# Kernel optimization log

Hardware: AMD Instinct MI355X
Metric: run time of the kernel (lower is better)

The kernel has to match this reference:

```python
import jax, jax.numpy as jnp
import numpy as np
from jax import lax

B, N, M = 4, 16384, 512
RADIUS2 = 4.0        # radius=2 (hard-coded in forward), compare squared distances
BALL_K = 64          # k=64 hard-coded in forward
KNN_K = 9            # opt.node_knn_k_1
SIGMA_LB = 0.001     # opt.loss_sigma_lower_bound

_DIMS = [("conv1", 6, 64), ("conv2", 64, 64), ("conv3", 64, 64),
         ("conv4", 128, 128), ("conv5", 128, 128),
         ("knnb1", 131, 256), ("knnb2", 256, 256), ("knnb3", 256, 256),
         ("knna1", 512, 512), ("knna2", 512, 512),
         ("mlp1", 640, 512), ("mlp2", 512, 256)]


def setup_inputs() -> dict:
    key = jax.random.key(0)
    ks = jax.random.split(key, 6)
    inp = {
        "x": jax.random.normal(ks[0], (B, 3, N), jnp.float32),
        "sn": jax.random.normal(ks[1], (B, 3, N), jnp.float32),
        "node": jax.random.normal(ks[2], (B, 3, M), jnp.float32),
    }
    for i, (name, cin, cout) in enumerate(_DIMS):
        k = jax.random.fold_in(ks[3], i)
        inp[name + "_w"] = jax.random.normal(k, (cout, cin), jnp.float32) * np.float32(1.0 / np.sqrt(cin))
        inp[name + "_b"] = jnp.zeros((cout,), jnp.float32)
    inp["mlp3_w"] = jax.random.normal(ks[4], (4, 256), jnp.float32) * np.float32(1e-4)  # .normal_(0, 0.0001)
    inp["mlp3_b"] = jnp.zeros((4,), jnp.float32)
    return inp


def _conv(f, w, b, act=True):
    # 1x1 conv over (B,C,M) or (B,C,M,K): channel matmul + bias (+relu)
    y = jnp.einsum('oc,bc...->bo...', w, f) + b.reshape((1, -1) + (1,) * (f.ndim - 2))
    return jax.nn.relu(y) if act else y


def _sqdist(a, b):
    # a: (B,3,Ma), b: (B,3,Nb) -> (B,Ma,Nb) squared euclidean distances
    aa = jnp.sum(a * a, axis=1)
    bb = jnp.sum(b * b, axis=1)
    ab = jnp.einsum('bcm,bcn->bmn', a, b)
    return aa[:, :, None] + bb[:, None, :] - 2.0 * ab


def _gather(feat, idx):
    # feat: (B,C,Nb), idx: (B,Mq,K) -> (B,C,Mq,K)
    Bq, C, _ = feat.shape
    _, Mq, K = idx.shape
    flat = jnp.broadcast_to(idx.reshape(Bq, 1, Mq * K), (Bq, C, Mq * K))
    return jnp.take_along_axis(feat, flat, axis=2).reshape(Bq, C, Mq, K)


def _ball_query(sqd, radius2, k):
    # first k point indices (in original order) with dist<radius, padded by the first hit
    n = sqd.shape[2]
    mask = sqd < radius2
    keyi = jnp.where(mask, jnp.arange(n, dtype=jnp.int32)[None, None, :], jnp.int32(n))
    _, idx = lax.top_k(-keyi, k)  # k smallest keys == first k in-ball indices
    count = jnp.sum(mask, axis=2, keepdims=True)
    return jnp.where(jnp.arange(k)[None, None, :] < count, idx, idx[:, :, :1])


def reference(x, sn, node,
              conv1_w, conv1_b, conv2_w, conv2_b, conv3_w, conv3_b,
              conv4_w, conv4_b, conv5_w, conv5_b,
              knnb1_w, knnb1_b, knnb2_w, knnb2_b, knnb3_w, knnb3_b,
              knna1_w, knna1_b, knna2_w, knna2_b,
              mlp1_w, mlp1_b, mlp2_w, mlp2_b, mlp3_w, mlp3_b):
    x_aug = jnp.concatenate([x, sn], axis=1)                      # (B,6,N)
    idx = _ball_query(_sqdist(node, x), RADIUS2, BALL_K)          # (B,M,64)
    xb = _gather(x_aug, idx)                                      # (B,6,M,64)
    xb = jnp.concatenate([xb[:, :3] - node[:, :, :, None], xb[:, 3:]], axis=1)
    f = _conv(_conv(_conv(xb, conv1_w, conv1_b), conv2_w, conv2_b), conv3_w, conv3_b)
    fmax = jnp.max(f, axis=3, keepdims=True)
    f = jnp.concatenate([f, jnp.broadcast_to(fmax, f.shape)], axis=1)
    f = _conv(_conv(f, conv4_w, conv4_b), conv5_w, conv5_b)
    feat1 = jnp.max(f, axis=3)                                    # (B,128,M)

    # GeneralKNNFusionModule: query=node, database=node, x=feat1, K=KNN_K
    _, knn_idx = lax.top_k(-_sqdist(node, node), KNN_K)           # (B,M,K) nearest nodes
    coords = _gather(node, knn_idx) - node[:, :, :, None]         # (B,3,M,K)
    g = jnp.concatenate([coords, _gather(feat1, knn_idx)], axis=1)  # (B,131,M,K)
    g = _conv(_conv(_conv(g, knnb1_w, knnb1_b), knnb2_w, knnb2_b), knnb3_w, knnb3_b)
    gmax = jnp.max(g, axis=3, keepdims=True)
    g = jnp.concatenate([g, jnp.broadcast_to(gmax, g.shape)], axis=1)
    g = _conv(_conv(g, knna1_w, knna1_b), knna2_w, knna2_b)
    feat2 = jnp.max(g, axis=3)                                    # (B,512,M)

    h = jnp.concatenate([feat1, feat2], axis=1)                   # (B,640,M)
    h = _conv(_conv(h, mlp1_w, mlp1_b), mlp2_w, mlp2_b)
    ksig = _conv(h, mlp3_w, mlp3_b, act=False)                    # (B,4,M)
    keypoints = ksig[:, :3] + node
    sigmas = jax.nn.softplus(ksig[:, 3]) + SIGMA_LB
    return node, keypoints, sigmas
```

## Files before the change

### kernel.cpp

```cpp
#include <hip/hip_runtime.h>

typedef unsigned short u16;
typedef unsigned int u32;
typedef __bf16 bf16x8 __attribute__((ext_vector_type(8)));
typedef float floatx4 __attribute__((ext_vector_type(4)));
typedef unsigned short u16x8 __attribute__((ext_vector_type(8)));
typedef unsigned int u32x4 __attribute__((ext_vector_type(4)));

static constexpr int B_ = 4;
static constexpr int N_ = 16384;
static constexpr int M_ = 512;

__device__ __forceinline__ u16 f2bf(float f) {
    u32 u = __float_as_uint(f);
    u32 r = (u + 0x7fffu + ((u >> 16) & 1u)) >> 16;
    return (u16)r;
}
__device__ __forceinline__ float bf2f(u16 x) {
    return __uint_as_float(((u32)x) << 16);
}
__device__ __forceinline__ u32 pack2(float a, float b) {
    return (u32)f2bf(a) | ((u32)f2bf(b) << 16);
}

struct WConvArgs { const float* src[12]; };

__global__ __launch_bounds__(256) void prep_kernel(
    const float* __restrict__ x, const float* __restrict__ node,
    int* __restrict__ idx, int* __restrict__ knn,
    WConvArgs wa, u16* __restrict__ Wbf) {
    int bid = blockIdx.x;
    int tid = threadIdx.x, wave = tid >> 6, lane = tid & 63;

    if (bid < 2048) {
        int bm = bid;
        int b = bm >> 9, m = bm & 511;
        __shared__ int sidx[4][64];
        __shared__ int scnt[4];
        const float* xb = x + (size_t)b * 3 * N_;
        float nx = node[((size_t)b * 3 + 0) * M_ + m];
        float ny = node[((size_t)b * 3 + 1) * M_ + m];
        float nz = node[((size_t)b * 3 + 2) * M_ + m];
        float aa = nx * nx + ny * ny + nz * nz;
        int cnt = 0;
        int base = wave * 4096;
        for (int n0 = base; n0 < base + 4096; n0 += 256) {
            float px[4], py[4], pz[4];
#pragma unroll
            for (int i = 0; i < 4; ++i) {
                int n = n0 + i * 64 + lane;
                px[i] = xb[n]; py[i] = xb[N_ + n]; pz[i] = xb[2 * N_ + n];
            }
#pragma unroll
            for (int i = 0; i < 4; ++i) {
                float bb = px[i] * px[i] + py[i] * py[i] + pz[i] * pz[i];
                float d = aa + bb - 2.0f * (nx * px[i] + ny * py[i] + nz * pz[i]);
                bool inb = d < 4.0f;
                unsigned long long mask = __ballot(inb);
                if (inb && cnt < 64) {
                    int pos = cnt + __popcll(mask & ((1ull << lane) - 1ull));
                    if (pos < 64) sidx[wave][pos] = n0 + i * 64 + lane;
                }
                cnt += __popcll(mask);
            }
            if (cnt >= 64) break;
        }
        if (lane == 0) scnt[wave] = cnt;
        __syncthreads();
        if (tid < 64) {
            int total = scnt[0] + scnt[1] + scnt[2] + scnt[3];
            int v = 0;
            if (total > 0) {
                int lim = total < 64 ? total : 64;
                int slot = tid < lim ? tid : 0;
                int w = 0, pre = 0;
                while (w < 3 && slot >= pre + scnt[w]) { pre += scnt[w]; ++w; }
                v = sidx[w][slot - pre];
            }
            idx[(size_t)bm * 64 + tid] = v;
        }
    } else if (bid < 2560) {
        int bm = (bid - 2048) * 4 + wave;
        int b = bm >> 9, m = bm & 511;
        const float* nb = node + (size_t)b * 3 * M_;
        float nx = nb[m], ny = nb[M_ + m], nz = nb[2 * M_ + m];
        float aa = nx * nx + ny * ny + nz * nz;
        float dist[8];
        int didx[8];
#pragma unroll
        for (int i = 0; i < 8; ++i) {
            int n = lane + i * 64;
            float px = nb[n], py = nb[M_ + n], pz = nb[2 * M_ + n];
            float bb = px * px + py * py + pz * pz;
            float ab = nx * px + ny * py + nz * pz;
            dist[i] = aa + bb - 2.0f * ab;
            didx[i] = n;
        }
        for (int r = 0; r < 9; ++r) {
            float bv = dist[0]; int bi = didx[0]; int bslot = 0;
#pragma unroll
            for (int i = 1; i < 8; ++i) {
                if (dist[i] < bv || (dist[i] == bv && didx[i] < bi)) {
                    bv = dist[i]; bi = didx[i]; bslot = i;
                }
            }
            float rv = bv; int ri = bi;
            for (int off = 32; off > 0; off >>= 1) {
                float ov = __shfl_down(rv, off);
                int   oi = __shfl_down(ri, off);
                if (ov < rv || (ov == rv && oi < ri)) { rv = ov; ri = oi; }
            }
            ri = __shfl(ri, 0);
            if (lane == 0) knn[(size_t)bm * 9 + r] = ri;
            if (bi == ri) dist[bslot] = 3.0e38f;
        }
    } else {
        const int CI[12] = {6, 64, 64, 128, 128, 131, 256, 256, 512, 512, 640, 512};
        const int KP[12] = {32, 64, 64, 128, 128, 160, 256, 256, 512, 512, 640, 512};
        const int OFF[13] = {0, 2048, 6144, 10240, 26624, 43008, 83968, 149504,
                             215040, 477184, 739328, 1067008, 1198080};
        int e = (bid - 2560) * 256 + tid;
        int w = 0;
        while (e >= OFF[w + 1]) ++w;
        int local = e - OFF[w];
        int kp = KP[w];
        int co = local / kp, k = local - co * kp;
        float v = 0.0f;
        if (w == 5) {
            if (k < 3) v = wa.src[5][(size_t)co * 131 + k];
            else if (k >= 8 && k < 136) v = wa.src[5][(size_t)co * 131 + (k - 5)];
        } else if (k < CI[w]) {
            v = wa.src[w][(size_t)co * CI[w] + k];
        }
        Wbf[e] = f2bf(v);
    }
}

static constexpr int RS = 136;

__device__ __forceinline__ bf16x8 ldsA(const u16* act, int rf, int l15, int quad, int ks) {
    return *(const bf16x8*)(act + (rf * 16 + l15) * RS + ks * 32 + quad * 8);
}
__device__ __forceinline__ bf16x8 ldW(const u16* W, int ks, int l15, int quad, int kstride) {
    return *(const bf16x8*)(W + (size_t)l15 * kstride + ks * 32 + quad * 8);
}

__global__ __launch_bounds__(256, 2) void fused_stage1_kernel(
    const float* __restrict__ x, const float* __restrict__ sn,
    const float* __restrict__ node, const int* __restrict__ idx,
    const u16* __restrict__ Wbf,
    const float* __restrict__ b1, const float* __restrict__ b2,
    const float* __restrict__ b3, const float* __restrict__ b4,
    const float* __restrict__ b5, u16* __restrict__ h) {
    __shared__ __align__(16) u16 act[256 * RS];
    __shared__ __align__(16) u16 mv[4][64];
    int blk = blockIdx.x;
    int bm0 = blk * 4;
    int tid = threadIdx.x, wave = tid >> 6, lane = tid & 63;
    int quad = lane >> 4, l15 = lane & 15;

    {
        int row = tid;
        int bm = bm0 + (row >> 6);
        int b = bm >> 9, m = bm & 511;
        int j = idx[(size_t)bm * 64 + (row & 63)];
        const float* xb = x + (size_t)b * 3 * N_;
        const float* sb = sn + (size_t)b * 3 * N_;
        float c0 = xb[j]          - node[((size_t)b * 3 + 0) * M_ + m];
        float c1 = xb[N_ + j]     - node[((size_t)b * 3 + 1) * M_ + m];
        float c2 = xb[2 * N_ + j] - node[((size_t)b * 3 + 2) * M_ + m];
        float s0 = sb[j], s1 = sb[N_ + j], s2 = sb[2 * N_ + j];
        u16* r = act + row * RS;
        *(u32*)(r)     = pack2(c0, c1);
        *(u32*)(r + 2) = pack2(c2, s0);
        *(u32*)(r + 4) = pack2(s1, s2);
        *(u32*)(r + 6) = 0u;
        u32x4* z = (u32x4*)(r + 8);
        z[0] = (u32x4){0u, 0u, 0u, 0u};
        z[1] = (u32x4){0u, 0u, 0u, 0u};
        z[2] = (u32x4){0u, 0u, 0u, 0u};
    }
    __syncthreads();

    {
        const u16* Wp = Wbf + (size_t)(wave * 16) * 32;
        bf16x8 bw = ldW(Wp, 0, l15, quad, 32);
        floatx4 c[16];
#pragma unroll
        for (int rf = 0; rf < 16; ++rf) {
            bf16x8 a = ldsA(act, rf, l15, quad, 0);
            c[rf] = __builtin_amdgcn_mfma_f32_16x16x32_bf16(a, bw, (floatx4){0.f,0.f,0.f,0.f}, 0, 0, 0);
        }
        float bias = b1[wave * 16 + l15];
        __syncthreads();
#pragma unroll
        for (int rf = 0; rf < 16; ++rf)
#pragma unroll
            for (int r = 0; r < 4; ++r)
                act[(rf * 16 + quad * 4 + r) * RS + wave * 16 + l15] = f2bf(fmaxf(c[rf][r] + bias, 0.0f));
        __syncthreads();
    }

    const int WOFF23[2] = {2048, 6144};
    const float* bp23[2] = {b2, b3};
#pragma unroll 1
    for (int cv = 0; cv < 2; ++cv) {
        const u16* Wp = Wbf + WOFF23[cv] + (size_t)(wave * 16) * 64;
        bf16x8 bw0 = ldW(Wp, 0, l15, quad, 64);
        bf16x8 bw1 = ldW(Wp, 1, l15, quad, 64);
        floatx4 c[16] = {};
#pragma unroll
        for (int ks = 0; ks < 2; ++ks)
#pragma unroll
            for (int rf = 0; rf < 16; ++rf) {
                bf16x8 a = ldsA(act, rf, l15, quad, ks);
                c[rf] = __builtin_amdgcn_mfma_f32_16x16x32_bf16(a, ks ? bw1 : bw0, c[rf], 0, 0, 0);
            }
        float bias = bp23[cv][wave * 16 + l15];
        float mxN[4] = {0.0f, 0.0f, 0.0f, 0.0f};
#pragma unroll
        for (int rf = 0; rf < 16; ++rf)
#pragma unroll
            for (int r = 0; r < 4; ++r) {
                float v = fmaxf(c[rf][r] + bias, 0.0f);
                mxN[rf >> 2] = fmaxf(mxN[rf >> 2], v);
            }
        __syncthreads();
#pragma unroll
        for (int rf = 0; rf < 16; ++rf)
#pragma unroll
            for (int r = 0; r < 4; ++r)
                act[(rf * 16 + quad * 4 + r) * RS + wave * 16 + l15] = f2bf(fmaxf(c[rf][r] + bias, 0.0f));
        if (cv == 1) {
#pragma unroll
            for (int n = 0; n < 4; ++n) {
                float mx = mxN[n];
                mx = fmaxf(mx, __shfl_xor(mx, 16));
                mx = fmaxf(mx, __shfl_xor(mx, 32));
                if (quad == 0) mv[n][wave * 16 + l15] = f2bf(mx);
            }
        }
        __syncthreads();
    }

    {
        const u16* Wp = Wbf + 10240 + (size_t)(wave * 32) * 128;
        bf16x8 bw[2][4];
#pragma unroll
        for (int cf = 0; cf < 2; ++cf)
#pragma unroll
            for (int ks = 0; ks < 4; ++ks)
                bw[cf][ks] = ldW(Wp + (size_t)cf * 16 * 128, ks, l15, quad, 128);
        floatx4 c[16][2] = {};
#pragma unroll
        for (int ks = 0; ks < 4; ++ks)
#pragma unroll
            for (int rf = 0; rf < 16; ++rf) {
                bf16x8 a = (ks < 2) ? ldsA(act, rf, l15, quad, ks)
                                    : *(const bf16x8*)(&mv[rf >> 2][(ks - 2) * 32 + quad * 8]);
#pragma unroll
                for (int cf = 0; cf < 2; ++cf)
                    c[rf][cf] = __builtin_amdgcn_mfma_f32_16x16x32_bf16(a, bw[cf][ks], c[rf][cf], 0, 0, 0);
            }
        float bias[2];
#pragma unroll
        for (int cf = 0; cf < 2; ++cf) bias[cf] = b4[wave * 32 + cf * 16 + l15];
        __syncthreads();
#pragma unroll
        for (int rf = 0; rf < 16; ++rf)
#pragma unroll
            for (int cf = 0; cf < 2; ++cf)
#pragma unroll
                for (int r = 0; r < 4; ++r)
                    act[(rf * 16 + quad * 4 + r) * RS + wave * 32 + cf * 16 + l15] =
                        f2bf(fmaxf(c[rf][cf][r] + bias[cf], 0.0f));
        __syncthreads();
    }

    {
        const u16* Wp = Wbf + 26624 + (size_t)(wave * 32) * 128;
        bf16x8 bw[2][4];
#pragma unroll
        for (int cf = 0; cf < 2; ++cf)
#pragma unroll
            for (int ks = 0; ks < 4; ++ks)
                bw[cf][ks] = ldW(Wp + (size_t)cf * 16 * 128, ks, l15, quad, 128);
        floatx4 c[16][2] = {};
#pragma unroll
        for (int ks = 0; ks < 4; ++ks)
#pragma unroll
            for (int rf = 0; rf < 16; ++rf) {
                bf16x8 a = ldsA(act, rf, l15, quad, ks);
#pragma unroll
                for (int cf = 0; cf < 2; ++cf)
                    c[rf][cf] = __builtin_amdgcn_mfma_f32_16x16x32_bf16(a, bw[cf][ks], c[rf][cf], 0, 0, 0);
            }
#pragma unroll
        for (int cf = 0; cf < 2; ++cf) {
            float bias = b5[wave * 32 + cf * 16 + l15];
            float mxN[4] = {0.0f, 0.0f, 0.0f, 0.0f};
#pragma unroll
            for (int rf = 0; rf < 16; ++rf)
#pragma unroll
                for (int r = 0; r < 4; ++r) {
                    float v = fmaxf(c[rf][cf][r] + bias, 0.0f);
                    mxN[rf >> 2] = fmaxf(mxN[rf >> 2], v);
                }
#pragma unroll
            for (int n = 0; n < 4; ++n) {
                float mx = mxN[n];
                mx = fmaxf(mx, __shfl_xor(mx, 16));
                mx = fmaxf(mx, __shfl_xor(mx, 32));
                if (quad == 0)
                    h[(size_t)(bm0 + n) * 640 + wave * 32 + cf * 16 + l15] = f2bf(mx);
            }
        }
    }
}

template <int KS, int CF, int RF, int PF, int RSx>
__device__ __forceinline__ void conv_inplace(u16* act, const u16* __restrict__ W0, int KP,
                                             const float* __restrict__ bias, int cb,
                                             int l15, int quad) {
    floatx4 acc[RF][CF];
#pragma unroll
    for (int rf = 0; rf < RF; ++rf)
#pragma unroll
        for (int cf = 0; cf < CF; ++cf) acc[rf][cf] = (floatx4){0.f, 0.f, 0.f, 0.f};

    bf16x8 bw[PF][CF];
#pragma unroll
    for (int p = 0; p < PF - 1; ++p)
        if (p < KS)
#pragma unroll
            for (int cf = 0; cf < CF; ++cf)
                bw[p][cf] = *(const bf16x8*)(W0 + (size_t)(cb + cf * 16 + l15) * KP +
                                             p * 32 + quad * 8);

#pragma unroll
    for (int ks = 0; ks < KS; ++ks) {
        if (ks + PF - 1 < KS) {
#pragma unroll
            for (int cf = 0; cf < CF; ++cf)
                bw[(ks + PF - 1) & (PF - 1)][cf] =
                    *(const bf16x8*)(W0 + (size_t)(cb + cf * 16 + l15) * KP +
                                     (ks + PF - 1) * 32 + quad * 8);
        }
#pragma unroll
        for (int rf = 0; rf < RF; ++rf) {
            bf16x8 a = *(const bf16x8*)(act + (rf * 16 + l15) * RSx + ks * 32 + quad * 8);
#pragma unroll
            for (int cf = 0; cf < CF; ++cf)
                acc[rf][cf] = __builtin_amdgcn_mfma_f32_16x16x32_bf16(a, bw[ks & (PF - 1)][cf], acc[rf][cf], 0, 0, 0);
        }
    }
    __syncthreads();
#pragma unroll
    for (int cf = 0; cf < CF; ++cf) {
        float bs = bias[cb + cf * 16 + l15];
#pragma unroll
        for (int rf = 0; rf < RF; ++rf)
#pragma unroll
            for (int r = 0; r < 4; ++r)
                act[(rf * 16 + quad * 4 + r) * RSx + cb + cf * 16 + l15] =
                    f2bf(fmaxf(acc[rf][cf][r] + bs, 0.0f));
    }
    __syncthreads();
}

static constexpr int RS2 = 520;
static constexpr int RS3 = 648;

__global__ __launch_bounds__(512, 2) void fused_stage23_kernel(
    const float* __restrict__ node, u16* __restrict__ h, const int* __restrict__ knn,
    const u16* __restrict__ Wbf,
    const float* __restrict__ bb1, const float* __restrict__ bb2,
    const float* __restrict__ bb3, const float* __restrict__ ba1,
    const float* __restrict__ ba2,
    const float* __restrict__ bm1, const float* __restrict__ bm2,
    const float* __restrict__ w3, const float* __restrict__ b3,
    float* __restrict__ out) {
    __shared__ __align__(16) u16 act[80 * RS2 + 16 * RS3];
    u16* mlpT = act + 80 * RS2;
    int blk = blockIdx.x;
    int node0 = blk * 8;
    int b = node0 >> 9;
    int tid = threadIdx.x, wave = tid >> 6, lane = tid & 63;
    int quad = lane >> 4, l15 = lane & 15;
    (void)lane;

    for (int e = tid; e < 80 * 20; e += 512)
        *(u16x8*)(act + (e / 20) * RS2 + (e % 20) * 8) = (u16x8){0,0,0,0,0,0,0,0};
    __syncthreads();
    for (int e = tid; e < 72 * 3; e += 512) {
        int r = e / 3, c = e - r * 3;
        int nodei = node0 + r / 9;
        int j = knn[(size_t)nodei * 9 + (r % 9)];
        float v = node[((size_t)b * 3 + c) * M_ + j] - node[((size_t)b * 3 + c) * M_ + (nodei & 511)];
        act[r * RS2 + c] = f2bf(v);
    }
    for (int e = tid; e < 72 * 16; e += 512) {
        int r = e >> 4, s = e & 15;
        int nodei = node0 + r / 9;
        int j = knn[(size_t)nodei * 9 + (r % 9)];
        *(u16x8*)(act + r * RS2 + 8 + s * 8) =
            *(const u16x8*)(h + (size_t)(b * 512 + j) * 640 + s * 8);
    }
    __syncthreads();

    conv_inplace<5, 2, 5, 4, RS2>(act, Wbf + 43008, 160, bb1, wave * 32, l15, quad);
    conv_inplace<8, 2, 5, 4, RS2>(act, Wbf + 83968, 256, bb2, wave * 32, l15, quad);
    conv_inplace<8, 2, 5, 4, RS2>(act, Wbf + 149504, 256, bb3, wave * 32, l15, quad);

    for (int e = tid; e < 8 * 32; e += 512) {
        int li = e >> 5, s = e & 31;
        int r0 = li * 9;
        float mx[8];
#pragma unroll
        for (int i = 0; i < 8; ++i) mx[i] = -3.0e38f;
#pragma unroll
        for (int kk = 0; kk < 9; ++kk) {
            u16x8 v = *(const u16x8*)(act + (r0 + kk) * RS2 + s * 8);
#pragma unroll
            for (int i = 0; i < 8; ++i) mx[i] = fmaxf(mx[i], bf2f(v[i]));
        }
        u16x8 o;
#pragma unroll
        for (int i = 0; i < 8; ++i) o[i] = f2bf(mx[i]);
#pragma unroll
        for (int kk = 0; kk < 9; ++kk)
            *(u16x8*)(act + (r0 + kk) * RS2 + 256 + s * 8) = o;
    }
    __syncthreads();

    conv_inplace<16, 4, 5, 4, RS2>(act, Wbf + 215040, 512, ba1, wave * 64, l15, quad);
    conv_inplace<16, 4, 5, 4, RS2>(act, Wbf + 477184, 512, ba2, wave * 64, l15, quad);

    for (int e = tid; e < 8 * 64; e += 512) {
        int li = e >> 6, s = e & 63;
        int r0 = li * 9;
        float mx[8];
#pragma unroll
        for (int i = 0; i < 8; ++i) mx[i] = -3.0e38f;
#pragma unroll
        for (int kk = 0; kk < 9; ++kk) {
            u16x8 v = *(const u16x8*)(act + (r0 + kk) * RS2 + s * 8);
#pragma unroll
            for (int i = 0; i < 8; ++i) mx[i] = fmaxf(mx[i], bf2f(v[i]));
        }
        u16x8 o;
#pragma unroll
        for (int i = 0; i < 8; ++i) o[i] = f2bf(mx[i]);
        *(u16x8*)(mlpT + li * RS3 + 128 + s * 8) = o;
    }
    for (int e = tid; e < 8 * 16; e += 512) {
        int li = e >> 4, s = e & 15;
        *(u16x8*)(mlpT + li * RS3 + s * 8) =
            *(const u16x8*)(h + (size_t)(node0 + li) * 640 + s * 8);
    }
    for (int e = tid; e < 8 * 80; e += 512) {
        int r = e / 80, seg = e - r * 80;
        *(u16x8*)(mlpT + (8 + r) * RS3 + seg * 8) = (u16x8){0,0,0,0,0,0,0,0};
    }
    __syncthreads();

    conv_inplace<20, 4, 1, 4, RS3>(mlpT, Wbf + 739328, 640, bm1, wave * 64, l15, quad);
    conv_inplace<16, 2, 1, 4, RS3>(mlpT, Wbf + 1067008, 512, bm2, wave * 32, l15, quad);

    if (tid < 32) {
        int li = tid >> 2, oc = tid & 3;
        const u16* row = mlpT + li * RS3;
        const float* wrow = w3 + oc * 256;
        float a = 0.0f;
        for (int c = 0; c < 256; c += 4) {
            a += bf2f(row[c]) * wrow[c];
            a += bf2f(row[c + 1]) * wrow[c + 1];
            a += bf2f(row[c + 2]) * wrow[c + 2];
            a += bf2f(row[c + 3]) * wrow[c + 3];
        }
        a += b3[oc];
        int nodei = node0 + li;
        int bo = nodei >> 9, m = nodei & 511;
        if (oc < 3) {
            float nv = node[((size_t)bo * 3 + oc) * M_ + m];
            out[((size_t)bo * 3 + oc) * M_ + m] = nv;
            out[6144 + ((size_t)bo * 3 + oc) * M_ + m] = nv + a;
        } else {
            out[12288 + nodei] = fmaxf(a, 0.0f) + log1pf(expf(-fabsf(a))) + 0.001f;
        }
    }
}

extern "C" void kernel_launch(void* const* d_in, const int* in_sizes, int n_in,
                              void* d_out, int out_size, void* d_ws, size_t ws_size,
                              hipStream_t stream) {
    (void)in_sizes; (void)n_in; (void)out_size; (void)ws_size;
    const float* x = (const float*)d_in[0];
    const float* sn = (const float*)d_in[1];
    const float* node = (const float*)d_in[2];
    const float* W[13];
    const float* Bs[13];
    for (int i = 0; i < 13; ++i) {
        W[i] = (const float*)d_in[3 + 2 * i];
        Bs[i] = (const float*)d_in[4 + 2 * i];
    }
    float* out = (float*)d_out;

    char* ws = (char*)d_ws;
    int* idx = (int*)(ws + 0);
    int* knn = (int*)(ws + 524288);
    u16* Wbf = (u16*)(ws + 598016);
    u16* h   = (u16*)(ws + 2994176);

    WConvArgs wa;
    for (int w = 0; w < 12; ++w) wa.src[w] = W[w];

    prep_kernel<<<7240, 256, 0, stream>>>(x, node, idx, knn, wa, Wbf);

    fused_stage1_kernel<<<512, 256, 0, stream>>>(x, sn, node, idx, Wbf,
                                                 Bs[0], Bs[1], Bs[2], Bs[3], Bs[4], h);
    fused_stage23_kernel<<<256, 512, 0, stream>>>(node, h, knn, Wbf,
                                                  Bs[5], Bs[6], Bs[7], Bs[8], Bs[9],
                                                  Bs[10], Bs[11], W[12], Bs[12], out);
}
```

Baseline: 222.7 us.

## Fuse ball query into stage1 and halve nodes per stage23 block

Moves the radius ball query out of the prep kernel and into the stage1 kernel. Each wave now scans points for its own node and writes neighbor indices to shared memory, so the idx workspace round trip goes away. The intermediate h buffer shrinks from 640 to 128 channels per node. Stage23 now handles 4 nodes per block instead of 8, with smaller shared memory, occupancy hint 4 and twice as many blocks. The cost is that a single wave scans the point list sequentially instead of four waves splitting it, which may lengthen the scan latency in stage1.

```diff
diff --git a/kernel.cpp b/kernel.cpp
--- a/kernel.cpp
+++ b/kernel.cpp
@@ -26,61 +26,13 @@
 struct WConvArgs { const float* src[12]; };
 
 __global__ __launch_bounds__(256) void prep_kernel(
-    const float* __restrict__ x, const float* __restrict__ node,
-    int* __restrict__ idx, int* __restrict__ knn,
+    const float* __restrict__ node, int* __restrict__ knn,
     WConvArgs wa, u16* __restrict__ Wbf) {
     int bid = blockIdx.x;
     int tid = threadIdx.x, wave = tid >> 6, lane = tid & 63;
 
-    if (bid < 2048) {
-        int bm = bid;
-        int b = bm >> 9, m = bm & 511;
-        __shared__ int sidx[4][64];
-        __shared__ int scnt[4];
-        const float* xb = x + (size_t)b * 3 * N_;
-        float nx = node[((size_t)b * 3 + 0) * M_ + m];
-        float ny = node[((size_t)b * 3 + 1) * M_ + m];
-        float nz = node[((size_t)b * 3 + 2) * M_ + m];
-        float aa = nx * nx + ny * ny + nz * nz;
-        int cnt = 0;
-        int base = wave * 4096;
-        for (int n0 = base; n0 < base + 4096; n0 += 256) {
-            float px[4], py[4], pz[4];
-#pragma unroll
-            for (int i = 0; i < 4; ++i) {
-                int n = n0 + i * 64 + lane;
-                px[i] = xb[n]; py[i] = xb[N_ + n]; pz[i] = xb[2 * N_ + n];
-            }
-#pragma unroll
-            for (int i = 0; i < 4; ++i) {
-                float bb = px[i] * px[i] + py[i] * py[i] + pz[i] * pz[i];
-                float d = aa + bb - 2.0f * (nx * px[i] + ny * py[i] + nz * pz[i]);
-                bool inb = d < 4.0f;
-                unsigned long long mask = __ballot(inb);
-                if (inb && cnt < 64) {
-                    int pos = cnt + __popcll(mask & ((1ull << lane) - 1ull));
-                    if (pos < 64) sidx[wave][pos] = n0 + i * 64 + lane;
-                }
-                cnt += __popcll(mask);
-            }
-            if (cnt >= 64) break;
-        }
-        if (lane == 0) scnt[wave] = cnt;
-        __syncthreads();
-        if (tid < 64) {
-            int total = scnt[0] + scnt[1] + scnt[2] + scnt[3];
-            int v = 0;
-            if (total > 0) {
-                int lim = total < 64 ? total : 64;
-                int slot = tid < lim ? tid : 0;
-                int w = 0, pre = 0;
-                while (w < 3 && slot >= pre + scnt[w]) { pre += scnt[w]; ++w; }
-                v = sidx[w][slot - pre];
-            }
-            idx[(size_t)bm * 64 + tid] = v;
-        }
-    } else if (bid < 2560) {
-        int bm = (bid - 2048) * 4 + wave;
+    if (bid < 512) {
+        int bm = bid * 4 + wave;
         int b = bm >> 9, m = bm & 511;
         const float* nb = node + (size_t)b * 3 * M_;
         float nx = nb[m], ny = nb[M_ + m], nz = nb[2 * M_ + m];
@@ -119,7 +71,7 @@
         const int KP[12] = {32, 64, 64, 128, 128, 160, 256, 256, 512, 512, 640, 512};
         const int OFF[13] = {0, 2048, 6144, 10240, 26624, 43008, 83968, 149504,
                              215040, 477184, 739328, 1067008, 1198080};
-        int e = (bid - 2560) * 256 + tid;
+        int e = (bid - 512) * 256 + tid;
         int w = 0;
         while (e >= OFF[w + 1]) ++w;
         int local = e - OFF[w];
@@ -147,23 +99,62 @@
 
 __global__ __launch_bounds__(256, 2) void fused_stage1_kernel(
     const float* __restrict__ x, const float* __restrict__ sn,
-    const float* __restrict__ node, const int* __restrict__ idx,
+    const float* __restrict__ node,
     const u16* __restrict__ Wbf,
     const float* __restrict__ b1, const float* __restrict__ b2,
     const float* __restrict__ b3, const float* __restrict__ b4,
     const float* __restrict__ b5, u16* __restrict__ h) {
     __shared__ __align__(16) u16 act[256 * RS];
     __shared__ __align__(16) u16 mv[4][64];
+    __shared__ int sidx[4][64];
+    __shared__ int scnt[4];
     int blk = blockIdx.x;
     int bm0 = blk * 4;
     int tid = threadIdx.x, wave = tid >> 6, lane = tid & 63;
     int quad = lane >> 4, l15 = lane & 15;
 
     {
+        int bm = bm0 + wave;
+        int b = bm >> 9, m = bm & 511;
+        const float* xb = x + (size_t)b * 3 * N_;
+        float nx = node[((size_t)b * 3 + 0) * M_ + m];
+        float ny = node[((size_t)b * 3 + 1) * M_ + m];
+        float nz = node[((size_t)b * 3 + 2) * M_ + m];
+        float aa = nx * nx + ny * ny + nz * nz;
+        int cnt = 0;
+#pragma unroll 1
+        for (int n0 = 0; n0 < N_; n0 += 256) {
+            float px[4], py[4], pz[4];
+#pragma unroll
+            for (int i = 0; i < 4; ++i) {
+                int n = n0 + i * 64 + lane;
+                px[i] = xb[n]; py[i] = xb[N_ + n]; pz[i] = xb[2 * N_ + n];
+            }
+#pragma unroll
+            for (int i = 0; i < 4; ++i) {
+                float bb = px[i] * px[i] + py[i] * py[i] + pz[i] * pz[i];
+                float d = aa + bb - 2.0f * (nx * px[i] + ny * py[i] + nz * pz[i]);
+                bool inb = d < 4.0f;
+                unsigned long long mask = __ballot(inb);
+                if (inb && cnt < 64) {
+                    int pos = cnt + __popcll(mask & ((1ull << lane) - 1ull));
+                    if (pos < 64) sidx[wave][pos] = n0 + i * 64 + lane;
+                }
+                cnt += __popcll(mask);
+            }
+            if (cnt >= 64) break;
+        }
+        if (lane == 0) scnt[wave] = cnt < 64 ? cnt : 64;
+    }
+    __syncthreads();
+
+    {
         int row = tid;
-        int bm = bm0 + (row >> 6);
+        int bm = bm0 + wave;
         int b = bm >> 9, m = bm & 511;
-        int j = idx[(size_t)bm * 64 + (row & 63)];
+        int c = scnt[wave];
+        int slot = row & 63;
+        int j = (c == 0) ? 0 : sidx[wave][slot < c ? slot : 0];
         const float* xb = x + (size_t)b * 3 * N_;
         const float* sb = sn + (size_t)b * 3 * N_;
         float c0 = xb[j]          - node[((size_t)b * 3 + 0) * M_ + m];
@@ -312,7 +303,7 @@
                 mx = fmaxf(mx, __shfl_xor(mx, 16));
                 mx = fmaxf(mx, __shfl_xor(mx, 32));
                 if (quad == 0)
-                    h[(size_t)(bm0 + n) * 640 + wave * 32 + cf * 16 + l15] = f2bf(mx);
+                    h[(size_t)(bm0 + n) * 128 + wave * 32 + cf * 16 + l15] = f2bf(mx);
             }
         }
     }
@@ -371,48 +362,55 @@
 static constexpr int RS2 = 520;
 static constexpr int RS3 = 648;
 
-__global__ __launch_bounds__(512, 2) void fused_stage23_kernel(
-    const float* __restrict__ node, u16* __restrict__ h, const int* __restrict__ knn,
-    const u16* __restrict__ Wbf,
+__global__ __launch_bounds__(512, 4) void fused_stage23_kernel(
+    const float* __restrict__ node, const u16* __restrict__ h,
+    const int* __restrict__ knn, const u16* __restrict__ Wbf,
     const float* __restrict__ bb1, const float* __restrict__ bb2,
     const float* __restrict__ bb3, const float* __restrict__ ba1,
     const float* __restrict__ ba2,
     const float* __restrict__ bm1, const float* __restrict__ bm2,
     const float* __restrict__ w3, const float* __restrict__ b3,
     float* __restrict__ out) {
-    __shared__ __align__(16) u16 act[80 * RS2 + 16 * RS3];
-    u16* mlpT = act + 80 * RS2;
+    __shared__ __align__(16) u16 act[48 * RS2];
+    u16* mlpT = act;
     int blk = blockIdx.x;
-    int node0 = blk * 8;
+    int node0 = blk * 4;
     int b = node0 >> 9;
     int tid = threadIdx.x, wave = tid >> 6, lane = tid & 63;
     int quad = lane >> 4, l15 = lane & 15;
     (void)lane;
 
-    for (int e = tid; e < 80 * 20; e += 512)
-        *(u16x8*)(act + (e / 20) * RS2 + (e % 20) * 8) = (u16x8){0,0,0,0,0,0,0,0};
-    __syncthreads();
-    for (int e = tid; e < 72 * 3; e += 512) {
-        int r = e / 3, c = e - r * 3;
+    if (tid < 36) {
+        int r = tid;
         int nodei = node0 + r / 9;
         int j = knn[(size_t)nodei * 9 + (r % 9)];
-        float v = node[((size_t)b * 3 + c) * M_ + j] - node[((size_t)b * 3 + c) * M_ + (nodei & 511)];
-        act[r * RS2 + c] = f2bf(v);
-    }
-    for (int e = tid; e < 72 * 16; e += 512) {
+        int m = nodei & 511;
+        float c0 = node[((size_t)b * 3 + 0) * M_ + j] - node[((size_t)b * 3 + 0) * M_ + m];
+        float c1 = node[((size_t)b * 3 + 1) * M_ + j] - node[((size_t)b * 3 + 1) * M_ + m];
+        float c2 = node[((size_t)b * 3 + 2) * M_ + j] - node[((size_t)b * 3 + 2) * M_ + m];
+        u16* rp = act + r * RS2;
+        *(u32*)(rp)     = pack2(c0, c1);
+        *(u32*)(rp + 2) = pack2(c2, 0.0f);
+        *(u32*)(rp + 4) = 0u;
+        *(u32*)(rp + 6) = 0u;
+        *(u16x8*)(rp + 136) = (u16x8){0,0,0,0,0,0,0,0};
+        *(u16x8*)(rp + 144) = (u16x8){0,0,0,0,0,0,0,0};
+        *(u16x8*)(rp + 152) = (u16x8){0,0,0,0,0,0,0,0};
+    }
+    for (int e = tid; e < 36 * 16; e += 512) {
         int r = e >> 4, s = e & 15;
         int nodei = node0 + r / 9;
         int j = knn[(size_t)nodei * 9 + (r % 9)];
         *(u16x8*)(act + r * RS2 + 8 + s * 8) =
-            *(const u16x8*)(h + (size_t)(b * 512 + j) * 640 + s * 8);
-    }
-    __syncthreads();
-
-    conv_inplace<5, 2, 5, 4, RS2>(act, Wbf + 43008, 160, bb1, wave * 32, l15, quad);
-    conv_inplace<8, 2, 5, 4, RS2>(act, Wbf + 83968, 256, bb2, wave * 32, l15, quad);
-    conv_inplace<8, 2, 5, 4, RS2>(act, Wbf + 149504, 256, bb3, wave * 32, l15, quad);
-
-    for (int e = tid; e < 8 * 32; e += 512) {
+            *(const u16x8*)(h + (size_t)(b * 512 + j) * 128 + s * 8);
+    }
+    __syncthreads();
+
+    conv_inplace<5, 2, 3, 4, RS2>(act, Wbf + 43008, 160, bb1, wave * 32, l15, quad);
+    conv_inplace<8, 2, 3, 4, RS2>(act, Wbf + 83968, 256, bb2, wave * 32, l15, quad);
+    conv_inplace<8, 2, 3, 4, RS2>(act, Wbf + 149504, 256, bb3, wave * 32, l15, quad);
+
+    for (int e = tid; e < 4 * 32; e += 512) {
         int li = e >> 5, s = e & 31;
         int r0 = li * 9;
         float mx[8];
@@ -433,41 +431,39 @@
     }
     __syncthreads();
 
-    conv_inplace<16, 4, 5, 4, RS2>(act, Wbf + 215040, 512, ba1, wave * 64, l15, quad);
-    conv_inplace<16, 4, 5, 4, RS2>(act, Wbf + 477184, 512, ba2, wave * 64, l15, quad);
-
-    for (int e = tid; e < 8 * 64; e += 512) {
-        int li = e >> 6, s = e & 63;
-        int r0 = li * 9;
+    conv_inplace<16, 4, 3, 4, RS2>(act, Wbf + 215040, 512, ba1, wave * 64, l15, quad);
+    conv_inplace<16, 4, 3, 4, RS2>(act, Wbf + 477184, 512, ba2, wave * 64, l15, quad);
+
+    u16x8 feat2o;
+    int pli = tid >> 6, ps = tid & 63;
+    if (tid < 256) {
+        int r0 = pli * 9;
         float mx[8];
 #pragma unroll
         for (int i = 0; i < 8; ++i) mx[i] = -3.0e38f;
 #pragma unroll
         for (int kk = 0; kk < 9; ++kk) {
-            u16x8 v = *(const u16x8*)(act + (r0 + kk) * RS2 + s * 8);
+            u16x8 v = *(const u16x8*)(act + (r0 + kk) * RS2 + ps * 8);
 #pragma unroll
             for (int i = 0; i < 8; ++i) mx[i] = fmaxf(mx[i], bf2f(v[i]));
         }
-        u16x8 o;
-#pragma unroll
-        for (int i = 0; i < 8; ++i) o[i] = f2bf(mx[i]);
-        *(u16x8*)(mlpT + li * RS3 + 128 + s * 8) = o;
-    }
-    for (int e = tid; e < 8 * 16; e += 512) {
-        int li = e >> 4, s = e & 15;
+#pragma unroll
+        for (int i = 0; i < 8; ++i) feat2o[i] = f2bf(mx[i]);
+    }
+    __syncthreads();
+    if (tid < 256)
+        *(u16x8*)(mlpT + pli * RS3 + 128 + ps * 8) = feat2o;
+    if (tid < 64) {
+        int li = tid >> 4, s = tid & 15;
         *(u16x8*)(mlpT + li * RS3 + s * 8) =
-            *(const u16x8*)(h + (size_t)(node0 + li) * 640 + s * 8);
-    }
-    for (int e = tid; e < 8 * 80; e += 512) {
-        int r = e / 80, seg = e - r * 80;
-        *(u16x8*)(mlpT + (8 + r) * RS3 + seg * 8) = (u16x8){0,0,0,0,0,0,0,0};
+            *(const u16x8*)(h + (size_t)(node0 + li) * 128 + s * 8);
     }
     __syncthreads();
 
     conv_inplace<20, 4, 1, 4, RS3>(mlpT, Wbf + 739328, 640, bm1, wave * 64, l15, quad);
     conv_inplace<16, 2, 1, 4, RS3>(mlpT, Wbf + 1067008, 512, bm2, wave * 32, l15, quad);
 
-    if (tid < 32) {
+    if (tid < 16) {
         int li = tid >> 2, oc = tid & 3;
         const u16* row = mlpT + li * RS3;
         const float* wrow = w3 + oc * 256;
@@ -507,19 +503,18 @@
     float* out = (float*)d_out;
 
     char* ws = (char*)d_ws;
-    int* idx = (int*)(ws + 0);
-    int* knn = (int*)(ws + 524288);
-    u16* Wbf = (u16*)(ws + 598016);
-    u16* h   = (u16*)(ws + 2994176);
+    int* knn = (int*)(ws + 0);
+    u16* Wbf = (u16*)(ws + 73728);
+    u16* h   = (u16*)(ws + 2469888);
 
     WConvArgs wa;
     for (int w = 0; w < 12; ++w) wa.src[w] = W[w];
 
-    prep_kernel<<<7240, 256, 0, stream>>>(x, node, idx, knn, wa, Wbf);
-
-    fused_stage1_kernel<<<512, 256, 0, stream>>>(x, sn, node, idx, Wbf,
+    prep_kernel<<<5192, 256, 0, stream>>>(node, knn, wa, Wbf);
+
+    fused_stage1_kernel<<<512, 256, 0, stream>>>(x, sn, node, Wbf,
                                                  Bs[0], Bs[1], Bs[2], Bs[3], Bs[4], h);
-    fused_stage23_kernel<<<256, 512, 0, stream>>>(node, h, knn, Wbf,
+    fused_stage23_kernel<<<512, 512, 0, stream>>>(node, h, knn, Wbf,
                                                   Bs[5], Bs[6], Bs[7], Bs[8], Bs[9],
                                                   Bs[10], Bs[11], W[12], Bs[12], out);
 }
```

Result: slower. 311.5 us (+39.9%).

## Fuse ball query into stage1 kernel with one node per block

Applied to the files above, without the earlier changes.

Moves the ball-query search from the prep kernel into the stage1 MLP kernel, so neighbour indices stay in shared memory instead of going through a global idx buffer. Stage1 now handles one node per block (2048 blocks, smaller LDS footprint, occupancy hint raised to 4), and the intermediate h buffer is compacted from a 640 to a 128 channel row stride. This removes a global round trip and raises parallelism, but the ball search now runs serially before the convs inside each block instead of in its own kernel.

```diff
diff --git a/kernel.cpp b/kernel.cpp
--- a/kernel.cpp
+++ b/kernel.cpp
@@ -26,61 +26,13 @@
 struct WConvArgs { const float* src[12]; };
 
 __global__ __launch_bounds__(256) void prep_kernel(
-    const float* __restrict__ x, const float* __restrict__ node,
-    int* __restrict__ idx, int* __restrict__ knn,
+    const float* __restrict__ node, int* __restrict__ knn,
     WConvArgs wa, u16* __restrict__ Wbf) {
     int bid = blockIdx.x;
     int tid = threadIdx.x, wave = tid >> 6, lane = tid & 63;
 
-    if (bid < 2048) {
-        int bm = bid;
-        int b = bm >> 9, m = bm & 511;
-        __shared__ int sidx[4][64];
-        __shared__ int scnt[4];
-        const float* xb = x + (size_t)b * 3 * N_;
-        float nx = node[((size_t)b * 3 + 0) * M_ + m];
-        float ny = node[((size_t)b * 3 + 1) * M_ + m];
-        float nz = node[((size_t)b * 3 + 2) * M_ + m];
-        float aa = nx * nx + ny * ny + nz * nz;
-        int cnt = 0;
-        int base = wave * 4096;
-        for (int n0 = base; n0 < base + 4096; n0 += 256) {
-            float px[4], py[4], pz[4];
-#pragma unroll
-            for (int i = 0; i < 4; ++i) {
-                int n = n0 + i * 64 + lane;
-                px[i] = xb[n]; py[i] = xb[N_ + n]; pz[i] = xb[2 * N_ + n];
-            }
-#pragma unroll
-            for (int i = 0; i < 4; ++i) {
-                float bb = px[i] * px[i] + py[i] * py[i] + pz[i] * pz[i];
-                float d = aa + bb - 2.0f * (nx * px[i] + ny * py[i] + nz * pz[i]);
-                bool inb = d < 4.0f;
-                unsigned long long mask = __ballot(inb);
-                if (inb && cnt < 64) {
-                    int pos = cnt + __popcll(mask & ((1ull << lane) - 1ull));
-                    if (pos < 64) sidx[wave][pos] = n0 + i * 64 + lane;
-                }
-                cnt += __popcll(mask);
-            }
-            if (cnt >= 64) break;
-        }
-        if (lane == 0) scnt[wave] = cnt;
-        __syncthreads();
-        if (tid < 64) {
-            int total = scnt[0] + scnt[1] + scnt[2] + scnt[3];
-            int v = 0;
-            if (total > 0) {
-                int lim = total < 64 ? total : 64;
-                int slot = tid < lim ? tid : 0;
-                int w = 0, pre = 0;
-                while (w < 3 && slot >= pre + scnt[w]) { pre += scnt[w]; ++w; }
-                v = sidx[w][slot - pre];
-            }
-            idx[(size_t)bm * 64 + tid] = v;
-        }
-    } else if (bid < 2560) {
-        int bm = (bid - 2048) * 4 + wave;
+    if (bid < 512) {
+        int bm = bid * 4 + wave;
         int b = bm >> 9, m = bm & 511;
         const float* nb = node + (size_t)b * 3 * M_;
         float nx = nb[m], ny = nb[M_ + m], nz = nb[2 * M_ + m];
@@ -119,7 +71,7 @@
         const int KP[12] = {32, 64, 64, 128, 128, 160, 256, 256, 512, 512, 640, 512};
         const int OFF[13] = {0, 2048, 6144, 10240, 26624, 43008, 83968, 149504,
                              215040, 477184, 739328, 1067008, 1198080};
-        int e = (bid - 2560) * 256 + tid;
+        int e = (bid - 512) * 256 + tid;
         int w = 0;
         while (e >= OFF[w + 1]) ++w;
         int local = e - OFF[w];
@@ -145,32 +97,73 @@
     return *(const bf16x8*)(W + (size_t)l15 * kstride + ks * 32 + quad * 8);
 }
 
-__global__ __launch_bounds__(256, 2) void fused_stage1_kernel(
+__global__ __launch_bounds__(256, 4) void fused_stage1_kernel(
     const float* __restrict__ x, const float* __restrict__ sn,
-    const float* __restrict__ node, const int* __restrict__ idx,
+    const float* __restrict__ node,
     const u16* __restrict__ Wbf,
     const float* __restrict__ b1, const float* __restrict__ b2,
     const float* __restrict__ b3, const float* __restrict__ b4,
     const float* __restrict__ b5, u16* __restrict__ h) {
-    __shared__ __align__(16) u16 act[256 * RS];
-    __shared__ __align__(16) u16 mv[4][64];
-    int blk = blockIdx.x;
-    int bm0 = blk * 4;
+    __shared__ __align__(16) u16 act[64 * RS];
+    __shared__ __align__(16) u16 mv[64];
+    __shared__ int sidx[4][64];
+    __shared__ int scnt[4];
+    int bm = blockIdx.x;
+    int b = bm >> 9, m = bm & 511;
     int tid = threadIdx.x, wave = tid >> 6, lane = tid & 63;
     int quad = lane >> 4, l15 = lane & 15;
 
     {
-        int row = tid;
-        int bm = bm0 + (row >> 6);
-        int b = bm >> 9, m = bm & 511;
-        int j = idx[(size_t)bm * 64 + (row & 63)];
+        const float* xb = x + (size_t)b * 3 * N_;
+        float nx = node[((size_t)b * 3 + 0) * M_ + m];
+        float ny = node[((size_t)b * 3 + 1) * M_ + m];
+        float nz = node[((size_t)b * 3 + 2) * M_ + m];
+        float aa = nx * nx + ny * ny + nz * nz;
+        int cnt = 0;
+        int base = wave * 4096;
+#pragma unroll 1
+        for (int n0 = base; n0 < base + 4096; n0 += 256) {
+            float px[4], py[4], pz[4];
+#pragma unroll
+            for (int i = 0; i < 4; ++i) {
+                int n = n0 + i * 64 + lane;
+                px[i] = xb[n]; py[i] = xb[N_ + n]; pz[i] = xb[2 * N_ + n];
+            }
+#pragma unroll
+            for (int i = 0; i < 4; ++i) {
+                float bb = px[i] * px[i] + py[i] * py[i] + pz[i] * pz[i];
+                float d = aa + bb - 2.0f * (nx * px[i] + ny * py[i] + nz * pz[i]);
+                bool inb = d < 4.0f;
+                unsigned long long mask = __ballot(inb);
+                if (inb && cnt < 64) {
+                    int pos = cnt + __popcll(mask & ((1ull << lane) - 1ull));
+                    if (pos < 64) sidx[wave][pos] = n0 + i * 64 + lane;
+                }
+                cnt += __popcll(mask);
+            }
+            if (cnt >= 64) break;
+        }
+        if (lane == 0) scnt[wave] = cnt;
+    }
+    __syncthreads();
+
+    if (tid < 64) {
+        int total = scnt[0] + scnt[1] + scnt[2] + scnt[3];
+        int j = 0;
+        if (total > 0) {
+            int lim = total < 64 ? total : 64;
+            int slot = tid < lim ? tid : 0;
+            int w = 0, pre = 0;
+            while (w < 3 && slot >= pre + scnt[w]) { pre += scnt[w]; ++w; }
+            j = sidx[w][slot - pre];
+        }
         const float* xb = x + (size_t)b * 3 * N_;
         const float* sb = sn + (size_t)b * 3 * N_;
         float c0 = xb[j]          - node[((size_t)b * 3 + 0) * M_ + m];
         float c1 = xb[N_ + j]     - node[((size_t)b * 3 + 1) * M_ + m];
         float c2 = xb[2 * N_ + j] - node[((size_t)b * 3 + 2) * M_ + m];
         float s0 = sb[j], s1 = sb[N_ + j], s2 = sb[2 * N_ + j];
-        u16* r = act + row * RS;
+        u16* r = act + tid * RS;
         *(u32*)(r)     = pack2(c0, c1);
         *(u32*)(r + 2) = pack2(c2, s0);
         *(u32*)(r + 4) = pack2(s1, s2);
@@ -185,16 +178,16 @@
     {
         const u16* Wp = Wbf + (size_t)(wave * 16) * 32;
         bf16x8 bw = ldW(Wp, 0, l15, quad, 32);
-        floatx4 c[16];
-#pragma unroll
-        for (int rf = 0; rf < 16; ++rf) {
+        floatx4 c[4];
+#pragma unroll
+        for (int rf = 0; rf < 4; ++rf) {
             bf16x8 a = ldsA(act, rf, l15, quad, 0);
             c[rf] = __builtin_amdgcn_mfma_f32_16x16x32_bf16(a, bw, (floatx4){0.f,0.f,0.f,0.f}, 0, 0, 0);
         }
         float bias = b1[wave * 16 + l15];
         __syncthreads();
 #pragma unroll
-        for (int rf = 0; rf < 16; ++rf)
+        for (int rf = 0; rf < 4; ++rf)
 #pragma unroll
             for (int r = 0; r < 4; ++r)
                 act[(rf * 16 + quad * 4 + r) * RS + wave * 16 + l15] = f2bf(fmaxf(c[rf][r] + bias, 0.0f));
@@ -208,37 +201,31 @@
         const u16* Wp = Wbf + WOFF23[cv] + (size_t)(wave * 16) * 64;
         bf16x8 bw0 = ldW(Wp, 0, l15, quad, 64);
         bf16x8 bw1 = ldW(Wp, 1, l15, quad, 64);
-        floatx4 c[16] = {};
+        floatx4 c[4] = {};
 #pragma unroll
         for (int ks = 0; ks < 2; ++ks)
 #pragma unroll
-            for (int rf = 0; rf < 16; ++rf) {
+            for (int rf = 0; rf < 4; ++rf) {
                 bf16x8 a = ldsA(act, rf, l15, quad, ks);
                 c[rf] = __builtin_amdgcn_mfma_f32_16x16x32_bf16(a, ks ? bw1 : bw0, c[rf], 0, 0, 0);
             }
         float bias = bp23[cv][wave * 16 + l15];
-        float mxN[4] = {0.0f, 0.0f, 0.0f, 0.0f};
-#pragma unroll
-        for (int rf = 0; rf < 16; ++rf)
-#pragma unroll
-            for (int r = 0; r < 4; ++r) {
-                float v = fmaxf(c[rf][r] + bias, 0.0f);
-                mxN[rf >> 2] = fmaxf(mxN[rf >> 2], v);
-            }
+        float mx = 0.0f;
+#pragma unroll
+        for (int rf = 0; rf < 4; ++rf)
+#pragma unroll
+            for (int r = 0; r < 4; ++r)
+                mx = fmaxf(mx, fmaxf(c[rf][r] + bias, 0.0f));
         __syncthreads();
 #pragma unroll
-        for (int rf = 0; rf < 16; ++rf)
+        for (int rf = 0; rf < 4; ++rf)
 #pragma unroll
             for (int r = 0; r < 4; ++r)
                 act[(rf * 16 + quad * 4 + r) * RS + wave * 16 + l15] = f2bf(fmaxf(c[rf][r] + bias, 0.0f));
         if (cv == 1) {
-#pragma unroll
-            for (int n = 0; n < 4; ++n) {
-                float mx = mxN[n];
-                mx = fmaxf(mx, __shfl_xor(mx, 16));
-                mx = fmaxf(mx, __shfl_xor(mx, 32));
-                if (quad == 0) mv[n][wave * 16 + l15] = f2bf(mx);
-            }
+            mx = fmaxf(mx, __shfl_xor(mx, 16));
+            mx = fmaxf(mx, __shfl_xor(mx, 32));
+            if (quad == 0) mv[wave * 16 + l15] = f2bf(mx);
         }
         __syncthreads();
     }
@@ -251,23 +238,25 @@
 #pragma unroll
             for (int ks = 0; ks < 4; ++ks)
                 bw[cf][ks] = ldW(Wp + (size_t)cf * 16 * 128, ks, l15, quad, 128);
-        floatx4 c[16][2] = {};
-#pragma unroll
-        for (int ks = 0; ks < 4; ++ks)
-#pragma unroll
-            for (int rf = 0; rf < 16; ++rf) {
-                bf16x8 a = (ks < 2) ? ldsA(act, rf, l15, quad, ks)
-                                    : *(const bf16x8*)(&mv[rf >> 2][(ks - 2) * 32 + quad * 8]);
+        floatx4 c[4][2] = {};
+#pragma unroll
+        for (int ks = 0; ks < 4; ++ks) {
+            bf16x8 amv;
+            if (ks >= 2) amv = *(const bf16x8*)(&mv[(ks - 2) * 32 + quad * 8]);
+#pragma unroll
+            for (int rf = 0; rf < 4; ++rf) {
+                bf16x8 a = (ks < 2) ? ldsA(act, rf, l15, quad, ks) : amv;
 #pragma unroll
                 for (int cf = 0; cf < 2; ++cf)
                     c[rf][cf] = __builtin_amdgcn_mfma_f32_16x16x32_bf16(a, bw[cf][ks], c[rf][cf], 0, 0, 0);
             }
+        }
         float bias[2];
 #pragma unroll
         for (int cf = 0; cf < 2; ++cf) bias[cf] = b4[wave * 32 + cf * 16 + l15];
         __syncthreads();
 #pragma unroll
-        for (int rf = 0; rf < 16; ++rf)
+        for (int rf = 0; rf < 4; ++rf)
 #pragma unroll
             for (int cf = 0; cf < 2; ++cf)
 #pragma unroll
@@ -285,11 +274,11 @@
 #pragma unroll
             for (int ks = 0; ks < 4; ++ks)
                 bw[cf][ks] = ldW(Wp + (size_t)cf * 16 * 128, ks, l15, quad, 128);
-        floatx4 c[16][2] = {};
+        floatx4 c[4][2] = {};
 #pragma unroll
         for (int ks = 0; ks < 4; ++ks)
 #pragma unroll
-            for (int rf = 0; rf < 16; ++rf) {
+            for (int rf = 0; rf < 4; ++rf) {
                 bf16x8 a = ldsA(act, rf, l15, quad, ks);
 #pragma unroll
                 for (int cf = 0; cf < 2; ++cf)
@@ -298,22 +287,16 @@
 #pragma unroll
         for (int cf = 0; cf < 2; ++cf) {
             float bias = b5[wave * 32 + cf * 16 + l15];
-            float mxN[4] = {0.0f, 0.0f, 0.0f, 0.0f};
-#pragma unroll
-            for (int rf = 0; rf < 16; ++rf)
-#pragma unroll
-                for (int r = 0; r < 4; ++r) {
-                    float v = fmaxf(c[rf][cf][r] + bias, 0.0f);
-                    mxN[rf >> 2] = fmaxf(mxN[rf >> 2], v);
-                }
-#pragma unroll
-            for (int n = 0; n < 4; ++n) {
-                float mx = mxN[n];
-                mx = fmaxf(mx, __shfl_xor(mx, 16));
-                mx = fmaxf(mx, __shfl_xor(mx, 32));
-                if (quad == 0)
-                    h[(size_t)(bm0 + n) * 640 + wave * 32 + cf * 16 + l15] = f2bf(mx);
-            }
+            float mx = 0.0f;
+#pragma unroll
+            for (int rf = 0; rf < 4; ++rf)
+#pragma unroll
+                for (int r = 0; r < 4; ++r)
+                    mx = fmaxf(mx, fmaxf(c[rf][cf][r] + bias, 0.0f));
+            mx = fmaxf(mx, __shfl_xor(mx, 16));
+            mx = fmaxf(mx, __shfl_xor(mx, 32));
+            if (quad == 0)
+                h[(size_t)bm * 128 + wave * 32 + cf * 16 + l15] = f2bf(mx);
         }
     }
 }
@@ -372,8 +355,8 @@
 static constexpr int RS3 = 648;
 
 __global__ __launch_bounds__(512, 2) void fused_stage23_kernel(
-    const float* __restrict__ node, u16* __restrict__ h, const int* __restrict__ knn,
-    const u16* __restrict__ Wbf,
+    const float* __restrict__ node, const u16* __restrict__ h,
+    const int* __restrict__ knn, const u16* __restrict__ Wbf,
     const float* __restrict__ bb1, const float* __restrict__ bb2,
     const float* __restrict__ bb3, const float* __restrict__ ba1,
     const float* __restrict__ ba2,
@@ -404,7 +387,7 @@
         int nodei = node0 + r / 9;
         int j = knn[(size_t)nodei * 9 + (r % 9)];
         *(u16x8*)(act + r * RS2 + 8 + s * 8) =
-            *(const u16x8*)(h + (size_t)(b * 512 + j) * 640 + s * 8);
+            *(const u16x8*)(h + (size_t)(b * 512 + j) * 128 + s * 8);
     }
     __syncthreads();
 
@@ -456,7 +439,7 @@
     for (int e = tid; e < 8 * 16; e += 512) {
         int li = e >> 4, s = e & 15;
         *(u16x8*)(mlpT + li * RS3 + s * 8) =
-            *(const u16x8*)(h + (size_t)(node0 + li) * 640 + s * 8);
+            *(const u16x8*)(h + (size_t)(node0 + li) * 128 + s * 8);
     }
     for (int e = tid; e < 8 * 80; e += 512) {
         int r = e / 80, seg = e - r * 80;
@@ -507,18 +490,17 @@
     float* out = (float*)d_out;
 
     char* ws = (char*)d_ws;
-    int* idx = (int*)(ws + 0);
-    int* knn = (int*)(ws + 524288);
-    u16* Wbf = (u16*)(ws + 598016);
-    u16* h   = (u16*)(ws + 2994176);
+    int* knn = (int*)(ws + 0);
+    u16* Wbf = (u16*)(ws + 73728);
+    u16* h   = (u16*)(ws + 2469888);
 
     WConvArgs wa;
     for (int w = 0; w < 12; ++w) wa.src[w] = W[w];
 
-    prep_kernel<<<7240, 256, 0, stream>>>(x, node, idx, knn, wa, Wbf);
-
-    fused_stage1_kernel<<<512, 256, 0, stream>>>(x, sn, node, idx, Wbf,
-                                                 Bs[0], Bs[1], Bs[2], Bs[3], Bs[4], h);
+    prep_kernel<<<5192, 256, 0, stream>>>(node, knn, wa, Wbf);
+
+    fused_stage1_kernel<<<2048, 256, 0, stream>>>(x, sn, node, Wbf,
+                                                  Bs[0], Bs[1], Bs[2], Bs[3], Bs[4], h);
     fused_stage23_kernel<<<256, 512, 0, stream>>>(node, h, knn, Wbf,
                                                   Bs[5], Bs[6], Bs[7], Bs[8], Bs[9],
                                                   Bs[10], Bs[11], W[12], Bs[12], out);
```

New measurement: 231.5 us. 4.0% more time.
